# Optimization experiments

Hardware: AMD Instinct MI355X
Metric: run time of the kernel (lower is better)

The kernel has to match this reference:

```python
import jax, jax.numpy as jnp
import numpy as np

DIM = 2
N_SIGMA = 2
THRESHOLD = 0.5
MIN_PIXEL = 160
MIN_INST_PIXEL = 160
MIN_SEED_THRESH = 0.5
INST_RATIO = 0.5
DIST_THRESH = 0.5
MAX_COUNT = 200


def setup_inputs() -> dict:
    key = jax.random.key(0)
    # scale 0.1 keeps sigma near 0 so exp(10*sigma)~O(1) and proposals are
    # realistically sized (same regime as a trained network's outputs).
    prediction = 0.1 * jax.random.normal(key, (1, 7, 1024, 2048), dtype=jnp.float32)
    return {"prediction": prediction}


def _forward(prediction):
    pred = prediction[0]                       # [C, H, W]
    H, W = pred.shape[1], pred.shape[2]
    # coordinate grid (larger=False: x in [0,2] over 2048, y in [0,1] over 1024)
    xm = jnp.linspace(0.0, 2.0, 2048)[:W]
    ym = jnp.linspace(0.0, 1.0, 1024)[:H]
    xym = jnp.stack([jnp.broadcast_to(xm[None, :], (H, W)),
                     jnp.broadcast_to(ym[:, None], (H, W))], axis=0)  # [2,H,W]

    spatial_emb = jnp.tanh(pred[0:DIM]) + xym               # [2,H,W]
    sigma = pred[DIM:DIM + N_SIGMA]                         # [2,H,W]
    seed = jax.nn.softmax(pred[DIM + 1 + N_SIGMA:DIM + N_SIGMA + 3], axis=0)[1]  # [H,W]

    N = H * W
    se = spatial_emb.reshape(DIM, N)
    sg = sigma.reshape(N_SIGMA, N)
    sm = seed.reshape(N)
    m = sm > MIN_SEED_THRESH                                # candidate-pixel mask

    unclustered0 = m.astype(jnp.float32)
    inst0 = jnp.zeros((N,), jnp.int32)
    prev0 = jnp.zeros((MAX_COUNT,), jnp.int32)              # proposal size at assignment time

    def cond(state):
        unclustered, inst, count, prev, stopped = state
        return (~stopped) & (jnp.sum(unclustered) > MIN_PIXEL) & (count < MAX_COUNT)

    def body(state):
        unclustered, inst, count, prev, stopped = state
        scores = sm * unclustered
        seed_idx = jnp.argmax(scores)
        seed_score = scores[seed_idx]
        stop_now = seed_score < THRESHOLD                   # == break in torch loop

        center = se[:, seed_idx]                            # [2]
        s = jnp.exp(sg[:, seed_idx] * 10.0)                 # [2]
        # exp(-sum((emb - center)^2 * s)) over all pixels; AND with mask m to
        # match torch (which only computes over masked pixels)
        dist = jnp.exp(-jnp.sum((se - center[:, None]) ** 2 * s[:, None], axis=0))
        proposal = (dist > DIST_THRESH) & m                 # [N] bool

        uncl = unclustered.at[seed_idx].set(0.0)            # unclustered[seed]=0
        prop_sum = jnp.sum(proposal)
        uncl_in_prop = jnp.sum(uncl * proposal)
        accept = (prop_sum > MIN_INST_PIXEL) & (
            uncl_in_prop / jnp.maximum(prop_sum.astype(jnp.float32), 1.0) > INST_RATIO)

        inst_new = jnp.where(accept & proposal, count, inst)
        prev_new = jnp.where(accept, prev.at[count].set(prop_sum), prev)
        count_new = jnp.where(accept, count + 1, count)
        uncl_new = jnp.where(proposal, 0.0, uncl)           # always consume proposal

        # if the seed score fell below threshold, revert and stop (break)
        return (jnp.where(stop_now, unclustered, uncl_new),
                jnp.where(stop_now, inst, inst_new),
                jnp.where(stop_now, count, count_new),
                jnp.where(stop_now, prev, prev_new),
                stop_now)

    state = (unclustered0, inst0, jnp.int32(1), prev0, jnp.array(False))
    unclustered, inst, count, prev, _ = jax.lax.while_loop(cond, body, state)

    # dropped if too small or too eroded
    now = jnp.bincount(inst, length=MAX_COUNT).astype(jnp.int32)
    ratio = now.astype(jnp.float32) / jnp.maximum(prev, 1).astype(jnp.float32)
    bad = (now != prev) & (now > 0) & ((now < MIN_INST_PIXEL * 3) | (ratio < INST_RATIO))
    bad = bad.at[0].set(False)                              # background never removed
    inst = jnp.where(bad[inst], 0, inst)
    return inst.reshape(H, W).astype(jnp.uint8)[None]       # [1,H,W]


def reference(prediction):
    return _forward(prediction)
```

## Files before the change

### kernel.cpp

```cpp
#include <hip/hip_runtime.h>
#include <cstddef>

typedef unsigned long long ull;

#define NPIX (1024 * 2048)
#define WW 2048
#define MAXC 200
#define GRIDB 256
#define BLKT 512
#define PXT 16
#define NW (BLKT / 64)
#define TAGSH 56
#define DMASK ((1ull << TAGSH) - 1)
#define TCAP 250

union F16x { float4 v[4]; float f[16]; };
union I16x { int4 v[4]; int f[16]; };

__device__ inline ull AL(ull* p) { return __hip_atomic_load(p, __ATOMIC_RELAXED, __HIP_MEMORY_SCOPE_AGENT); }
__device__ inline void AS(ull* p, ull v) { __hip_atomic_store(p, v, __ATOMIC_RELAXED, __HIP_MEMORY_SCOPE_AGENT); }
__device__ inline void ASI(int* p, int v) { __hip_atomic_store(p, v, __ATOMIC_RELAXED, __HIP_MEMORY_SCOPE_AGENT); }
__device__ inline int ALI(int* p) { return __hip_atomic_load(p, __ATOMIC_RELAXED, __HIP_MEMORY_SCOPE_AGENT); }

__device__ inline ull shfl_down_u64(ull v, int o) {
  unsigned lo = (unsigned)v, hi = (unsigned)(v >> 32);
  lo = __shfl_down(lo, o, 64);
  hi = __shfl_down(hi, o, 64);
  return ((ull)hi << 32) | lo;
}
__device__ inline void wred_kz(ull& k, ull& z) {
  #pragma unroll
  for (int o = 32; o > 0; o >>= 1) {
    ull k2 = shfl_down_u64(k, o), z2 = shfl_down_u64(z, o);
    if (k2 > k) k = k2;
    z += z2;
  }
}

__global__ __launch_bounds__(BLKT, 1) void k_all(
    const float* __restrict__ pred,
    ull* __restrict__ slots,
    int* __restrict__ prevp, int* __restrict__ nowp,
    int* __restrict__ out)
{
  __shared__ ull lsaK[4], lsaZ[4];
  __shared__ ull lsbK[NW], lsbZ[NW];
  __shared__ int lbad[MAXC];

  const int b = blockIdx.x, tid = threadIdx.x;
  const int wid = tid >> 6, lane = tid & 63;
  const int base = (b * BLKT + tid) * PXT;
  const float dxs = 2.0f / 2047.0f;
  const float dys = 1.0f / 1023.0f;

  F16x Av, Bv, Sv;
  ull iv0 = 0, iv1 = 0;
  unsigned pp = 0;

  {
    F16x P, Q;
    const int h = base >> 11, wb = base & (WW - 1);
    const float yv = __fmul_rn((float)h, dys);
    #pragma unroll
    for (int q = 0; q < 4; q++) P.v[q] = *(const float4*)(pred + base + 4 * q);
    #pragma unroll
    for (int j = 0; j < PXT; j++)
      Av.f[j] = __fadd_rn(tanhf(P.f[j]), __fmul_rn((float)(wb + j), dxs));
    #pragma unroll
    for (int q = 0; q < 4; q++) P.v[q] = *(const float4*)(pred + NPIX + base + 4 * q);
    #pragma unroll
    for (int j = 0; j < PXT; j++)
      Bv.f[j] = __fadd_rn(tanhf(P.f[j]), yv);
    #pragma unroll
    for (int q = 0; q < 4; q++) P.v[q] = *(const float4*)(pred + 5 * NPIX + base + 4 * q);
    #pragma unroll
    for (int q = 0; q < 4; q++) Q.v[q] = *(const float4*)(pred + 6 * NPIX + base + 4 * q);
    #pragma unroll
    for (int j = 0; j < PXT; j++) {
      float a = P.f[j], bb = Q.f[j];
      float mx = fmaxf(a, bb);
      float ea = expf(__fsub_rn(a, mx));
      float eb = expf(__fsub_rn(bb, mx));
      Sv.f[j] = __fdiv_rn(eb, __fadd_rn(ea, eb));
    }
    ull bk = 0; int cnt = 0;
    #pragma unroll
    for (int j = 0; j < PXT; j++) {
      float s = Sv.f[j];
      cnt += (s > 0.5f) ? 1 : 0;
      float sc = (s > 0.5f) ? s : 0.0f;
      ull pk = ((ull)__float_as_uint(sc) << 21) | (ull)(0x1FFFFFu - (unsigned)(base + j));
      if (pk > bk) bk = pk;
    }
    ull bz = ((ull)(unsigned)cnt) << 24;
    wred_kz(bk, bz);
    if (lane == 0) { lsbK[wid] = bk; lsbZ[wid] = bz; }
    if (b == 0)
      for (int c = tid; c < MAXC; c += BLKT) { ASI(&nowp[c], 0); ASI(&prevp[c], 0); }
    __syncthreads();
    if (tid == 0) {
      ull K = lsbK[0], Z = lsbZ[0];
      for (int i = 1; i < NW; i++) { if (lsbK[i] > K) K = lsbK[i]; Z += lsbZ[i]; }
      const ull tw = 1ull << TAGSH;
      AS(&slots[b * 8 + 1], tw | Z);
      AS(&slots[b * 8 + 0], tw | K);
    }
  }

  int count = 1, rem = 0, tstop = 0;
  for (int t = 0;; ++t) {
    const unsigned tg = (unsigned)(t + 1) & 0xFFu;
    if (tid < GRIDB) {
      ull* sl = &slots[tid * 8];
      ull k, z;
      for (;;) {
        k = AL(sl); z = AL(sl + 1);
        if (((unsigned)(k >> TAGSH) == tg) & ((unsigned)(z >> TAGSH) == tg)) break;
      }
      k &= DMASK; z &= DMASK;
      wred_kz(k, z);
      if (lane == 0) { lsaK[wid] = k; lsaZ[wid] = z; }
    }
    __syncthreads();
    ull K = lsaK[0], Z = lsaZ[0];
    #pragma unroll
    for (int i = 1; i < 4; i++) { ull kk = lsaK[i]; if (kk > K) K = kk; Z += lsaZ[i]; }

    bool accP = false; int labP = 0;
    if (t == 0) {
      rem = (int)(Z >> 24);
    } else {
      int ps = (int)((Z >> 24) & 0xFFFFFF), ui = (int)(Z & 0xFFFFFF);
      accP = (ps > 160) &&
             (__fdiv_rn((float)(ui - 1), fmaxf((float)ps, 1.0f)) > 0.5f);
      if (accP) {
        labP = count;
        if (b == 0 && tid == 0) ASI(&prevp[count], ps);
        count++;
      }
      rem -= ui;
    }
    if (accP && pp) {
      #pragma unroll
      for (int j = 0; j < 8; j++)
        if ((pp >> j) & 1) iv0 = (iv0 & ~(0xFFull << (8 * j))) | ((ull)(unsigned)labP << (8 * j));
      #pragma unroll
      for (int j = 0; j < 8; j++)
        if ((pp >> (8 + j)) & 1) iv1 = (iv1 & ~(0xFFull << (8 * j))) | ((ull)(unsigned)labP << (8 * j));
    }
    if (!((rem > 160) && (count < MAXC))) { tstop = t; break; }
    const float score = __uint_as_float((unsigned)((K >> 21) & 0x7FFFFFFF));
    if (score < 0.5f) { tstop = t; break; }
    const int sidx = 0x1FFFFF - (int)(K & 0x1FFFFF);

    const float p0 = pred[sidx];
    const float p1 = pred[NPIX + sidx];
    const float p2 = pred[2 * NPIX + sidx];
    const float p3 = pred[3 * NPIX + sidx];
    const float c0 = __fadd_rn(tanhf(p0), __fmul_rn((float)(sidx & (WW - 1)), dxs));
    const float c1 = __fadd_rn(tanhf(p1), __fmul_rn((float)(sidx >> 11), dys));
    const float s0 = expf(__fmul_rn(p2, 10.0f));
    const float s1 = expf(__fmul_rn(p3, 10.0f));

    ull bk = 0; int psl = 0, uil = 0; unsigned ppn = 0;
    #pragma unroll
    for (int j = 0; j < PXT; j++) {
      float d0 = __fsub_rn(Av.f[j], c0);
      float d1 = __fsub_rn(Bv.f[j], c1);
      float tt = __fadd_rn(__fmul_rn(__fmul_rn(d0, d0), s0),
                           __fmul_rn(__fmul_rn(d1, d1), s1));
      float dist = expf(-tt);
      float s = Sv.f[j];
      bool pr = (dist > 0.5f) && (fabsf(s) > 0.5f);
      if (pr) {
        ppn |= 1u << j;
        psl++;
        if (s > 0.5f) { uil++; s = -s; Sv.f[j] = s; }
      }
      float sc = (s > 0.5f) ? s : 0.0f;
      ull pk = ((ull)__float_as_uint(sc) << 21) | (ull)(0x1FFFFFu - (unsigned)(base + j));
      if (pk > bk) bk = pk;
    }
    pp = ppn;
    ull bz = ((ull)(unsigned)psl << 24) | (unsigned)uil;
    wred_kz(bk, bz);
    if (lane == 0) { lsbK[wid] = bk; lsbZ[wid] = bz; }
    __syncthreads();
    if (tid == 0) {
      ull K2 = lsbK[0], Z2 = lsbZ[0];
      for (int i = 1; i < NW; i++) { if (lsbK[i] > K2) K2 = lsbK[i]; Z2 += lsbZ[i]; }
      const ull tw = ((ull)((unsigned)(t + 2) & 0xFFu)) << TAGSH;
      AS(&slots[b * 8 + 1], tw | Z2);
      AS(&slots[b * 8 + 0], tw | K2);
    }
    if (t + 1 >= TCAP) { tstop = t + 1; break; }
  }

  for (int c = tid; c < MAXC; c += BLKT) lbad[c] = 0;
  __syncthreads();
  {
    int cur = -1, acc = 0;
    #pragma unroll
    for (int j = 0; j < PXT; j++) {
      int lb = (int)(((j < 8) ? (iv0 >> (8 * j)) : (iv1 >> (8 * (j - 8)))) & 0xFF);
      if (lb == cur) acc++;
      else { if (cur > 0) atomicAdd(&lbad[cur], acc); cur = lb; acc = 1; }
    }
    if (cur > 0) atomicAdd(&lbad[cur], acc);
  }
  __syncthreads();
  for (int c = tid + 1; c < MAXC; c += BLKT)
    if (lbad[c]) atomicAdd(&nowp[c], lbad[c]);
  __syncthreads();
  {
    const unsigned etg = (unsigned)(tstop + 2) & 0xFFu;
    if (tid == 0)
      __hip_atomic_store(&slots[b * 8], ((ull)etg) << TAGSH,
                         __ATOMIC_RELEASE, __HIP_MEMORY_SCOPE_AGENT);
    if (tid < GRIDB) {
      ull* sl = &slots[tid * 8];
      while ((unsigned)(__hip_atomic_load(sl, __ATOMIC_ACQUIRE,
                                          __HIP_MEMORY_SCOPE_AGENT) >> TAGSH) != etg) {}
    }
  }
  __syncthreads();
  if (tid < MAXC) {
    int c = tid;
    int nw = (c == 0) ? 0 : ALI(&nowp[c]);
    int pv = ALI(&prevp[c]);
    float ratio = __fdiv_rn((float)nw, (float)(pv > 1 ? pv : 1));
    int bd = (nw != pv) && (nw > 0) && ((nw < 3 * 160) || (ratio < 0.5f));
    if (c == 0) bd = 0;
    lbad[c] = bd;
  }
  __syncthreads();
  {
    I16x O;
    #pragma unroll
    for (int j = 0; j < PXT; j++) {
      int v = (int)(((j < 8) ? (iv0 >> (8 * j)) : (iv1 >> (8 * (j - 8)))) & 0xFF);
      O.f[j] = lbad[v] ? 0 : v;
    }
    #pragma unroll
    for (int q = 0; q < 4; q++) *(int4*)(out + base + 4 * q) = O.v[q];
  }
}

extern "C" void kernel_launch(void* const* d_in, const int* in_sizes, int n_in,
                              void* d_out, int out_size, void* d_ws, size_t ws_size,
                              hipStream_t stream) {
  const float* pred = (const float*)d_in[0];
  char* ws = (char*)d_ws;
  size_t off = 0;
  ull* slots = (ull*)(ws + off); off += (size_t)GRIDB * 8 * sizeof(ull);
  int* prevp = (int*)(ws + off); off += MAXC * sizeof(int);
  int* nowp  = (int*)(ws + off); off += MAXC * sizeof(int);
  int* out = (int*)d_out;

  hipLaunchKernelGGL(k_all, dim3(GRIDB), dim3(BLKT), 0, stream,
                     pred, slots, prevp, nowp, out);
}
```

Measured before the change: 53.07 us.

## Publish winning seed parameters via slots and skip exp in the distance test

Each iteration, the thread that owns the block's best seed now publishes that seed's center and sigma values to the block's slot entries. Every block then reads them from the winning block's slot instead of doing four dependent global loads and transcendental calls from pred, falling back to recomputing them after a bounded spin. Block size doubles to 1024 threads with 8 pixels per thread, and the per-pixel exp in the distance test becomes a threshold compare on the exponent, calling exp only near the boundary. Per-thread argmax now tracks a float score and index instead of packed 64-bit compares. The TCAP iteration cap is removed, and more threads per block means larger intra-block reductions on the serial critical path.

```diff
diff --git a/kernel.cpp b/kernel.cpp
--- a/kernel.cpp
+++ b/kernel.cpp
@@ -7,15 +7,14 @@
 #define WW 2048
 #define MAXC 200
 #define GRIDB 256
-#define BLKT 512
-#define PXT 16
+#define BLKT 1024
+#define PXT 8
 #define NW (BLKT / 64)
 #define TAGSH 56
 #define DMASK ((1ull << TAGSH) - 1)
-#define TCAP 250
-
-union F16x { float4 v[4]; float f[16]; };
-union I16x { int4 v[4]; int f[16]; };
+
+union F8 { float4 v[2]; float f[8]; };
+union I8 { int4 v[2]; int f[8]; };
 
 __device__ inline ull AL(ull* p) { return __hip_atomic_load(p, __ATOMIC_RELAXED, __HIP_MEMORY_SCOPE_AGENT); }
 __device__ inline void AS(ull* p, ull v) { __hip_atomic_store(p, v, __ATOMIC_RELAXED, __HIP_MEMORY_SCOPE_AGENT); }
@@ -36,8 +35,16 @@
     z += z2;
   }
 }
-
-__global__ __launch_bounds__(BLKT, 1) void k_all(
+__device__ inline float sel8(const F8& x, int j) {
+  const float4 lo = x.v[0], hi = x.v[1];
+  float hx = (j & 4) ? hi.x : lo.x, hy = (j & 4) ? hi.y : lo.y;
+  float hz = (j & 4) ? hi.z : lo.z, hw = (j & 4) ? hi.w : lo.w;
+  float a = (j & 2) ? hz : hx;
+  float c = (j & 2) ? hw : hy;
+  return (j & 1) ? c : a;
+}
+
+__global__ __launch_bounds__(BLKT) void k_all(
     const float* __restrict__ pred,
     ull* __restrict__ slots,
     int* __restrict__ prevp, int* __restrict__ nowp,
@@ -49,32 +56,31 @@
 
   const int b = blockIdx.x, tid = threadIdx.x;
   const int wid = tid >> 6, lane = tid & 63;
-  const int base = (b * BLKT + tid) * PXT;
+  const int gtid = b * BLKT + tid;
+  const int base = gtid * PXT;
   const float dxs = 2.0f / 2047.0f;
   const float dys = 1.0f / 1023.0f;
 
-  F16x Av, Bv, Sv;
-  ull iv0 = 0, iv1 = 0;
+  F8 Av, Bv, Sv, R2, R3;
+  ull iv = 0;
   unsigned pp = 0;
 
   {
-    F16x P, Q;
+    F8 P, Q;
     const int h = base >> 11, wb = base & (WW - 1);
     const float yv = __fmul_rn((float)h, dys);
-    #pragma unroll
-    for (int q = 0; q < 4; q++) P.v[q] = *(const float4*)(pred + base + 4 * q);
+    P.v[0] = *(const float4*)(pred + base);     P.v[1] = *(const float4*)(pred + base + 4);
     #pragma unroll
     for (int j = 0; j < PXT; j++)
       Av.f[j] = __fadd_rn(tanhf(P.f[j]), __fmul_rn((float)(wb + j), dxs));
-    #pragma unroll
-    for (int q = 0; q < 4; q++) P.v[q] = *(const float4*)(pred + NPIX + base + 4 * q);
+    P.v[0] = *(const float4*)(pred + NPIX + base); P.v[1] = *(const float4*)(pred + NPIX + base + 4);
     #pragma unroll
     for (int j = 0; j < PXT; j++)
       Bv.f[j] = __fadd_rn(tanhf(P.f[j]), yv);
-    #pragma unroll
-    for (int q = 0; q < 4; q++) P.v[q] = *(const float4*)(pred + 5 * NPIX + base + 4 * q);
-    #pragma unroll
-    for (int q = 0; q < 4; q++) Q.v[q] = *(const float4*)(pred + 6 * NPIX + base + 4 * q);
+    R2.v[0] = *(const float4*)(pred + 2 * NPIX + base); R2.v[1] = *(const float4*)(pred + 2 * NPIX + base + 4);
+    R3.v[0] = *(const float4*)(pred + 3 * NPIX + base); R3.v[1] = *(const float4*)(pred + 3 * NPIX + base + 4);
+    P.v[0] = *(const float4*)(pred + 5 * NPIX + base); P.v[1] = *(const float4*)(pred + 5 * NPIX + base + 4);
+    Q.v[0] = *(const float4*)(pred + 6 * NPIX + base); Q.v[1] = *(const float4*)(pred + 6 * NPIX + base + 4);
     #pragma unroll
     for (int j = 0; j < PXT; j++) {
       float a = P.f[j], bb = Q.f[j];
@@ -83,32 +89,39 @@
       float eb = expf(__fsub_rn(bb, mx));
       Sv.f[j] = __fdiv_rn(eb, __fadd_rn(ea, eb));
     }
-    ull bk = 0; int cnt = 0;
+    float bsc = 0.0f; int bj = 0, cnt = 0;
     #pragma unroll
     for (int j = 0; j < PXT; j++) {
       float s = Sv.f[j];
-      cnt += (s > 0.5f) ? 1 : 0;
-      float sc = (s > 0.5f) ? s : 0.0f;
-      ull pk = ((ull)__float_as_uint(sc) << 21) | (ull)(0x1FFFFFu - (unsigned)(base + j));
-      if (pk > bk) bk = pk;
-    }
+      bool mm = s > 0.5f;
+      cnt += mm ? 1 : 0;
+      float sc = mm ? s : 0.0f;
+      if (sc > bsc) { bsc = sc; bj = j; }
+    }
+    ull bk = ((ull)__float_as_uint(bsc) << 21) | (ull)(0x1FFFFFu - (unsigned)(base + bj));
     ull bz = ((ull)(unsigned)cnt) << 24;
     wred_kz(bk, bz);
     if (lane == 0) { lsbK[wid] = bk; lsbZ[wid] = bz; }
     if (b == 0)
       for (int c = tid; c < MAXC; c += BLKT) { ASI(&nowp[c], 0); ASI(&prevp[c], 0); }
     __syncthreads();
-    if (tid == 0) {
-      ull K = lsbK[0], Z = lsbZ[0];
-      for (int i = 1; i < NW; i++) { if (lsbK[i] > K) K = lsbK[i]; Z += lsbZ[i]; }
-      const ull tw = 1ull << TAGSH;
-      AS(&slots[b * 8 + 1], tw | Z);
-      AS(&slots[b * 8 + 0], tw | K);
-    }
+    ull K = lsbK[0], Z = lsbZ[0];
+    #pragma unroll
+    for (int i = 1; i < NW; i++) { ull kk = lsbK[i]; if (kk > K) K = kk; Z += lsbZ[i]; }
+    const ull tw = 1ull << TAGSH;
+    const int bsidx = 0x1FFFFF - (int)(K & 0x1FFFFF);
+    if ((bsidx >> 3) == gtid) {
+      const int j = bsidx & 7;
+      AS(&slots[b * 8 + 2], tw | __float_as_uint(sel8(Av, j)));
+      AS(&slots[b * 8 + 3], tw | __float_as_uint(sel8(Bv, j)));
+      AS(&slots[b * 8 + 4], tw | __float_as_uint(expf(__fmul_rn(sel8(R2, j), 10.0f))));
+      AS(&slots[b * 8 + 5], tw | __float_as_uint(expf(__fmul_rn(sel8(R3, j), 10.0f))));
+    }
+    if (tid == 0) { AS(&slots[b * 8 + 1], tw | Z); AS(&slots[b * 8 + 0], tw | K); }
   }
 
   int count = 1, rem = 0, tstop = 0;
-  for (int t = 0;; ++t) {
+  for (int t = 0; t < (1 << 20); ++t) {
     const unsigned tg = (unsigned)(t + 1) & 0xFFu;
     if (tid < GRIDB) {
       ull* sl = &slots[tid * 8];
@@ -125,6 +138,10 @@
     ull K = lsaK[0], Z = lsaZ[0];
     #pragma unroll
     for (int i = 1; i < 4; i++) { ull kk = lsaK[i]; if (kk > K) K = kk; Z += lsaZ[i]; }
+    const int sidx = 0x1FFFFF - (int)(K & 0x1FFFFF);
+    const int winb = sidx >> 13;
+    ull* wp = &slots[(ull)winb * 8 + 2];
+    ull w2 = AL(wp), w3 = AL(wp + 1), w4 = AL(wp + 2), w5 = AL(wp + 3);
 
     bool accP = false; int labP = 0;
     if (t == 0) {
@@ -142,58 +159,76 @@
     }
     if (accP && pp) {
       #pragma unroll
-      for (int j = 0; j < 8; j++)
-        if ((pp >> j) & 1) iv0 = (iv0 & ~(0xFFull << (8 * j))) | ((ull)(unsigned)labP << (8 * j));
-      #pragma unroll
-      for (int j = 0; j < 8; j++)
-        if ((pp >> (8 + j)) & 1) iv1 = (iv1 & ~(0xFFull << (8 * j))) | ((ull)(unsigned)labP << (8 * j));
+      for (int j = 0; j < PXT; j++)
+        if ((pp >> j) & 1) iv = (iv & ~(0xFFull << (8 * j))) | ((ull)(unsigned)labP << (8 * j));
     }
     if (!((rem > 160) && (count < MAXC))) { tstop = t; break; }
     const float score = __uint_as_float((unsigned)((K >> 21) & 0x7FFFFFFF));
     if (score < 0.5f) { tstop = t; break; }
-    const int sidx = 0x1FFFFF - (int)(K & 0x1FFFFF);
-
-    const float p0 = pred[sidx];
-    const float p1 = pred[NPIX + sidx];
-    const float p2 = pred[2 * NPIX + sidx];
-    const float p3 = pred[3 * NPIX + sidx];
-    const float c0 = __fadd_rn(tanhf(p0), __fmul_rn((float)(sidx & (WW - 1)), dxs));
-    const float c1 = __fadd_rn(tanhf(p1), __fmul_rn((float)(sidx >> 11), dys));
-    const float s0 = expf(__fmul_rn(p2, 10.0f));
-    const float s1 = expf(__fmul_rn(p3, 10.0f));
-
-    ull bk = 0; int psl = 0, uil = 0; unsigned ppn = 0;
-    #pragma unroll
-    for (int j = 0; j < PXT; j++) {
+
+    float c0, c1, s0, s1;
+    {
+      bool ok; int spins = 0;
+      for (;;) {
+        ok = ((unsigned)(w2 >> TAGSH) == tg) & ((unsigned)(w3 >> TAGSH) == tg) &
+             ((unsigned)(w4 >> TAGSH) == tg) & ((unsigned)(w5 >> TAGSH) == tg);
+        if (ok || ++spins >= 512) break;
+        w2 = AL(wp); w3 = AL(wp + 1); w4 = AL(wp + 2); w5 = AL(wp + 3);
+      }
+      if (ok) {
+        c0 = __uint_as_float((unsigned)w2); c1 = __uint_as_float((unsigned)w3);
+        s0 = __uint_as_float((unsigned)w4); s1 = __uint_as_float((unsigned)w5);
+      } else {
+        const float p0 = pred[sidx], p1 = pred[NPIX + sidx];
+        const float p2 = pred[2 * NPIX + sidx], p3 = pred[3 * NPIX + sidx];
+        c0 = __fadd_rn(tanhf(p0), __fmul_rn((float)(sidx & (WW - 1)), dxs));
+        c1 = __fadd_rn(tanhf(p1), __fmul_rn((float)(sidx >> 11), dys));
+        s0 = expf(__fmul_rn(p2, 10.0f));
+        s1 = expf(__fmul_rn(p3, 10.0f));
+      }
+    }
+
+    float bsc = 0.0f; int bj = 0, psl = 0, uil = 0; unsigned ppn = 0;
+    #pragma unroll
+    for (int j = 0; j < PXT; j++) {
+      float s = Sv.f[j];
       float d0 = __fsub_rn(Av.f[j], c0);
       float d1 = __fsub_rn(Bv.f[j], c1);
       float tt = __fadd_rn(__fmul_rn(__fmul_rn(d0, d0), s0),
                            __fmul_rn(__fmul_rn(d1, d1), s1));
-      float dist = expf(-tt);
-      float s = Sv.f[j];
-      bool pr = (dist > 0.5f) && (fabsf(s) > 0.5f);
+      bool dok = (tt <= 0.693120f);
+      if (__builtin_expect((!dok) && (tt < 0.693175f), 0))
+        dok = (expf(-tt) > 0.5f);
+      bool pr = dok && (fabsf(s) > 0.5f);
       if (pr) {
         ppn |= 1u << j;
         psl++;
         if (s > 0.5f) { uil++; s = -s; Sv.f[j] = s; }
       }
       float sc = (s > 0.5f) ? s : 0.0f;
-      ull pk = ((ull)__float_as_uint(sc) << 21) | (ull)(0x1FFFFFu - (unsigned)(base + j));
-      if (pk > bk) bk = pk;
+      if (sc > bsc) { bsc = sc; bj = j; }
     }
     pp = ppn;
+    ull bk = ((ull)__float_as_uint(bsc) << 21) | (ull)(0x1FFFFFu - (unsigned)(base + bj));
     ull bz = ((ull)(unsigned)psl << 24) | (unsigned)uil;
     wred_kz(bk, bz);
     if (lane == 0) { lsbK[wid] = bk; lsbZ[wid] = bz; }
     __syncthreads();
-    if (tid == 0) {
+    {
       ull K2 = lsbK[0], Z2 = lsbZ[0];
-      for (int i = 1; i < NW; i++) { if (lsbK[i] > K2) K2 = lsbK[i]; Z2 += lsbZ[i]; }
+      #pragma unroll
+      for (int i = 1; i < NW; i++) { ull kk = lsbK[i]; if (kk > K2) K2 = kk; Z2 += lsbZ[i]; }
       const ull tw = ((ull)((unsigned)(t + 2) & 0xFFu)) << TAGSH;
-      AS(&slots[b * 8 + 1], tw | Z2);
-      AS(&slots[b * 8 + 0], tw | K2);
-    }
-    if (t + 1 >= TCAP) { tstop = t + 1; break; }
+      const int bsidx = 0x1FFFFF - (int)(K2 & 0x1FFFFF);
+      if ((bsidx >> 3) == gtid) {
+        const int j = bsidx & 7;
+        AS(&slots[b * 8 + 2], tw | __float_as_uint(sel8(Av, j)));
+        AS(&slots[b * 8 + 3], tw | __float_as_uint(sel8(Bv, j)));
+        AS(&slots[b * 8 + 4], tw | __float_as_uint(expf(__fmul_rn(sel8(R2, j), 10.0f))));
+        AS(&slots[b * 8 + 5], tw | __float_as_uint(expf(__fmul_rn(sel8(R3, j), 10.0f))));
+      }
+      if (tid == 0) { AS(&slots[b * 8 + 1], tw | Z2); AS(&slots[b * 8 + 0], tw | K2); }
+    }
   }
 
   for (int c = tid; c < MAXC; c += BLKT) lbad[c] = 0;
@@ -202,7 +237,7 @@
     int cur = -1, acc = 0;
     #pragma unroll
     for (int j = 0; j < PXT; j++) {
-      int lb = (int)(((j < 8) ? (iv0 >> (8 * j)) : (iv1 >> (8 * (j - 8)))) & 0xFF);
+      int lb = (int)((iv >> (8 * j)) & 0xFF);
       if (lb == cur) acc++;
       else { if (cur > 0) atomicAdd(&lbad[cur], acc); cur = lb; acc = 1; }
     }
@@ -235,14 +270,14 @@
   }
   __syncthreads();
   {
-    I16x O;
-    #pragma unroll
-    for (int j = 0; j < PXT; j++) {
-      int v = (int)(((j < 8) ? (iv0 >> (8 * j)) : (iv1 >> (8 * (j - 8)))) & 0xFF);
+    I8 O;
+    #pragma unroll
+    for (int j = 0; j < PXT; j++) {
+      int v = (int)((iv >> (8 * j)) & 0xFF);
       O.f[j] = lbad[v] ? 0 : v;
     }
-    #pragma unroll
-    for (int q = 0; q < 4; q++) *(int4*)(out + base + 4 * q) = O.v[q];
+    *(int4*)(out + base) = O.v[0];
+    *(int4*)(out + base + 4) = O.v[1];
   }
 }
 
```

Measured after the change: 58.37 us. 10.0% more time.
